# Optimization experiments

Hardware: AMD Instinct MI355X
Metric: run time of the kernel (lower is better)

The kernel has to match this reference:

```python
import jax, jax.numpy as jnp
import numpy as np

N = 50000      # nodes
E = 400000     # edges
IN = 128       # in_dim == emb_dim (residual requires equality)
POS = 64       # pos_in_dim
EMB = 128
LN_EPS = 1e-5


def _ln(x, g, b):
    m = jnp.mean(x, axis=-1, keepdims=True)
    v = jnp.mean((x - m) ** 2, axis=-1, keepdims=True)
    return (x - m) / jnp.sqrt(v + LN_EPS) * g + b


def _gin(x, src, dst, eps, W1, b1, g1, be1, W2, b2):
    # GINConv: mlp((1+eps)*x + sum_{j in N(i)} x_j)
    agg = jax.ops.segment_sum(x[src], dst, num_segments=x.shape[0])
    h = (1.0 + eps) * x + agg
    h = jax.nn.relu(_ln(h @ W1 + b1, g1, be1))
    return h @ W2 + b2


def setup_inputs() -> dict:
    key = jax.random.key(0)
    ks = jax.random.split(key, 8)
    x = jax.random.normal(ks[0], (N, IN), jnp.float32)
    pos = jax.random.normal(ks[1], (N, POS), jnp.float32)
    edge_index = jax.random.randint(ks[2], (2, E), 0, N)
    d = IN + POS
    f32 = jnp.float32
    W1 = (jax.random.normal(ks[3], (d, EMB), f32) / np.sqrt(d))
    W2 = (jax.random.normal(ks[4], (EMB, EMB), f32) / np.sqrt(EMB))
    W1p = (jax.random.normal(ks[5], (POS, EMB), f32) / np.sqrt(POS))
    W2p = (jax.random.normal(ks[6], (EMB, EMB), f32) / np.sqrt(EMB))
    z = jnp.zeros((EMB,), f32)
    o = jnp.ones((EMB,), f32)
    return {
        "x": x, "pos": pos, "edge_index": edge_index,
        "eps": jnp.zeros((), f32), "W1": W1, "b1": z, "g1": o, "be1": z,
        "W2": W2, "b2": z, "ln_g": o, "ln_b": z,
        "epsp": jnp.zeros((), f32), "W1p": W1p, "b1p": z, "g1p": o, "be1p": z,
        "W2p": W2p, "b2p": z, "lnp_g": o, "lnp_b": z,
    }


def reference(x, pos, edge_index, eps, W1, b1, g1, be1, W2, b2, ln_g, ln_b,
              epsp, W1p, b1p, g1p, be1p, W2p, b2p, lnp_g, lnp_b):
    src, dst = edge_index[0], edge_index[1]
    node_feats = jnp.concatenate([x, pos], axis=-1)  # [N, IN+POS]
    h = jax.nn.relu(_ln(_gin(node_feats, src, dst, eps, W1, b1, g1, be1, W2, b2), ln_g, ln_b))
    p = jax.nn.relu(_ln(_gin(pos, src, dst, epsp, W1p, b1p, g1p, be1p, W2p, b2p), lnp_g, lnp_b))
    # dropout is identity in eval mode (model_drop_ratio applied only when training)
    h = h + x  # add_residual=True
    return (h, p)
```

## Files before the change

### kernel.cpp

```cpp
#include <hip/hip_runtime.h>

#define NN    50000
#define NPAD  50048
#define HB    391
#define EE    400000
#define IND   128
#define POSD  64
#define DD    192
#define EMBD  128
#define LNEPS 1e-5f
#define CAP   32

#define CAT_B  4692
#define FILL_B 98
#define FILLV_B 391
#define WC_B   256

typedef __attribute__((ext_vector_type(8))) short bf16x8;
typedef __attribute__((ext_vector_type(4))) unsigned short u16x4;
typedef __attribute__((ext_vector_type(4))) float f32x4;
typedef unsigned short ushort_t;
typedef unsigned int uint_t;

#define MFMA16 __builtin_amdgcn_mfma_f32_16x16x32_bf16

__device__ inline ushort_t f2bf(float f) {
  union { float f; unsigned u; } v; v.f = f;
  unsigned r = (v.u + 0x7FFFu + ((v.u >> 16) & 1u)) >> 16;
  return (ushort_t)r;
}
__device__ inline float bf2f(unsigned u) {
  union { unsigned u; float f; } v; v.u = u << 16;
  return v.f;
}

__global__ __launch_bounds__(256) void prep_k(
    const float* __restrict__ x, const float* __restrict__ pos,
    const int* __restrict__ ei,
    const float* __restrict__ W1, const float* __restrict__ W2,
    const float* __restrict__ W1p, const float* __restrict__ W2p,
    int* __restrict__ cnt, int* __restrict__ csr,
    ushort_t* __restrict__ cat, ushort_t* __restrict__ wt) {
  const int bid = blockIdx.x;
  if (bid < FILLV_B) {
    int e0 = (bid * 256 + threadIdx.x) * 4;
    if (e0 >= EE) return;
    int4 s = *(const int4*)(ei + e0);
    int4 d = *(const int4*)(ei + EE + e0);
    int i0 = atomicAdd(&cnt[d.x], 1);
    int i1 = atomicAdd(&cnt[d.y], 1);
    int i2 = atomicAdd(&cnt[d.z], 1);
    int i3 = atomicAdd(&cnt[d.w], 1);
    if (i0 < CAP) csr[(size_t)d.x * CAP + i0] = s.x;
    if (i1 < CAP) csr[(size_t)d.y * CAP + i1] = s.y;
    if (i2 < CAP) csr[(size_t)d.z * CAP + i2] = s.z;
    if (i3 < CAP) csr[(size_t)d.w * CAP + i3] = s.w;
  } else if (bid < FILLV_B + CAT_B) {
    int id  = (bid - FILLV_B) * 256 + threadIdx.x;
    int n   = id / 24, sub = id - n * 24;
    bf16x8 o = (bf16x8){0, 0, 0, 0, 0, 0, 0, 0};
    if (n < NN) {
      const float* src = (sub < 16) ? (x + (size_t)n * IND + sub * 8)
                                    : (pos + (size_t)n * POSD + (sub - 16) * 8);
      f32x4 v0 = *(const f32x4*)(src);
      f32x4 v1 = *(const f32x4*)(src + 4);
#pragma unroll
      for (int i = 0; i < 4; ++i) {
        o[i]     = (short)f2bf(v0[i]);
        o[i + 4] = (short)f2bf(v1[i]);
      }
    }
    *(bf16x8*)(cat + (size_t)n * DD + sub * 8) = o;
  } else {
    int t = (bid - FILLV_B - CAT_B) * 256 + threadIdx.x;
    if (t < 24576) {
      int c = t / 192, k = t % 192;
      wt[t] = f2bf(W1[k * EMBD + c]);
    } else if (t < 40960) {
      int q = t - 24576; int c = q / 128, k = q % 128;
      wt[t] = f2bf(W2[k * EMBD + c]);
    } else if (t < 49152) {
      int q = t - 40960; int c = q / 64, k = q % 64;
      wt[t] = f2bf(W1p[k * EMBD + c]);
    } else {
      int q = t - 49152; int c = q / 128, k = q % 128;
      wt[t] = f2bf(W2p[k * EMBD + c]);
    }
  }
}

__global__ __launch_bounds__(256) void gather2_k(
    const ushort_t* __restrict__ cat, const int* __restrict__ cnt,
    const int* __restrict__ csr,
    const float* __restrict__ epsv, const float* __restrict__ epspv,
    ushort_t* __restrict__ h0, ushort_t* __restrict__ p0) {
  const int lane = threadIdx.x & 63;
  const int wv   = threadIdx.x >> 6;
  const int half = lane >> 5;
  const int l2   = lane & 31;
  const int n    = blockIdx.x * 8 + wv * 2 + half;

  int deg = 0;
  if (n < NN) { deg = cnt[n]; if (deg > CAP) deg = CAP; }
  int idx = (l2 < deg) ? csr[(size_t)n * CAP + l2] : NN;

  float a0 = 0.f, a1 = 0.f, a2 = 0.f, a3 = 0.f, a4 = 0.f, a5 = 0.f;
  for (int t = 0; t < deg; t += 8) {
    int s[8];
#pragma unroll
    for (int k = 0; k < 8; ++k) s[k] = __shfl(idx, half * 32 + t + k);
    u16x4 u[8]; uint_t v[8];
#pragma unroll
    for (int k = 0; k < 8; ++k) {
      int sk = (t + k < CAP) ? s[k] : NN;
      const ushort_t* r = cat + (size_t)sk * DD;
      u[k] = *(const u16x4*)(r + l2 * 4);
      v[k] = *(const uint_t*)(r + 128 + l2 * 2);
    }
#pragma unroll
    for (int k = 0; k < 8; ++k) {
      a0 += bf2f(u[k][0]); a1 += bf2f(u[k][1]);
      a2 += bf2f(u[k][2]); a3 += bf2f(u[k][3]);
      a4 += bf2f(v[k] & 0xffffu); a5 += bf2f(v[k] >> 16);
    }
  }

  const float e1  = 1.0f + epsv[0];
  const float ep1 = 1.0f + epspv[0];
  const ushort_t* self = cat + (size_t)n * DD;
  u16x4 su = *(const u16x4*)(self + l2 * 4);
  uint_t sv = *(const uint_t*)(self + 128 + l2 * 2);

  u16x4 o;
  o[0] = f2bf(fmaf(e1, bf2f(su[0]), a0));
  o[1] = f2bf(fmaf(e1, bf2f(su[1]), a1));
  o[2] = f2bf(fmaf(e1, bf2f(su[2]), a2));
  o[3] = f2bf(fmaf(e1, bf2f(su[3]), a3));
  *(u16x4*)(h0 + (size_t)n * DD + l2 * 4) = o;

  float p4 = bf2f(sv & 0xffffu), p5 = bf2f(sv >> 16);
  uint_t oh = (uint_t)f2bf(fmaf(e1, p4, a4)) |
              ((uint_t)f2bf(fmaf(e1, p5, a5)) << 16);
  *(uint_t*)(h0 + (size_t)n * DD + 128 + l2 * 2) = oh;
  uint_t op = (uint_t)f2bf(fmaf(ep1, p4, a4)) |
              ((uint_t)f2bf(fmaf(ep1, p5, a5)) << 16);
  *(uint_t*)(p0 + (size_t)n * POSD + l2 * 2) = op;
}

__device__ inline void ln_epi_T(f32x4 (&acc)[8][2],
                                const float* __restrict__ bias,
                                const float* __restrict__ gam,
                                const float* __restrict__ bet, int g) {
  f32x4 bv[8], gv[8], bev[8];
#pragma unroll
  for (int nt = 0; nt < 8; ++nt) {
    bv[nt]  = *(const f32x4*)(bias + nt * 16 + g * 4);
    gv[nt]  = *(const f32x4*)(gam  + nt * 16 + g * 4);
    bev[nt] = *(const f32x4*)(bet  + nt * 16 + g * 4);
  }
#pragma unroll
  for (int mt = 0; mt < 2; ++mt) {
    float s = 0.f, sq = 0.f;
#pragma unroll
    for (int nt = 0; nt < 8; ++nt)
#pragma unroll
      for (int r = 0; r < 4; ++r) {
        float v = acc[nt][mt][r] + bv[nt][r];
        acc[nt][mt][r] = v;
        s += v; sq += v * v;
      }
    s  += __shfl_xor(s, 16);  sq += __shfl_xor(sq, 16);
    s  += __shfl_xor(s, 32);  sq += __shfl_xor(sq, 32);
    float mean = s * (1.0f / 128.0f);
    float var  = sq * (1.0f / 128.0f) - mean * mean;
    float rstd = rsqrtf(var + LNEPS);
#pragma unroll
    for (int nt = 0; nt < 8; ++nt)
#pragma unroll
      for (int r = 0; r < 4; ++r)
        acc[nt][mt][r] = fmaxf(
            fmaf((acc[nt][mt][r] - mean) * rstd, gv[nt][r], bev[nt][r]), 0.f);
  }
}

__device__ inline void act_write_T(char* act, f32x4 (&acc)[8][2], int g, int c0) {
#pragma unroll
  for (int mt = 0; mt < 2; ++mt) {
    int lr = mt * 16 + c0;
    int sw = (lr & 7) << 4;
#pragma unroll
    for (int nt = 0; nt < 8; ++nt) {
      u16x4 o;
#pragma unroll
      for (int r = 0; r < 4; ++r) o[r] = f2bf(acc[nt][mt][r]);
      *(u16x4*)(act + lr * 256 + ((nt * 32 + g * 8) ^ sw)) = o;
    }
  }
}

__device__ inline void stage_w(const ushort_t* __restrict__ src, char* dst,
                               int rowbytes, int chunks, int tid) {
  int cpr = rowbytes >> 4;
  for (int i = tid; i < chunks; i += 256) {
    int row  = i / cpr;
    int colb = (i - row * cpr) << 4;
    *(bf16x8*)(dst + row * rowbytes + (colb ^ ((row & 7) << 4))) =
        *(const bf16x8*)(src + (size_t)i * 8);
  }
}

__global__ __launch_bounds__(256) void mlp_k(
    const ushort_t* __restrict__ h0, const ushort_t* __restrict__ p0,
    const ushort_t* __restrict__ wt,
    const float* __restrict__ b1, const float* __restrict__ g1,
    const float* __restrict__ be1,
    const float* __restrict__ b2, const float* __restrict__ lng,
    const float* __restrict__ lnb,
    const float* __restrict__ b1p, const float* __restrict__ g1p,
    const float* __restrict__ be1p,
    const float* __restrict__ b2p, const float* __restrict__ lnpg,
    const float* __restrict__ lnpb,
    const float* __restrict__ x, float* __restrict__ out) {
  __shared__ __align__(16) char smem[65536];
  const int tid  = threadIdx.x;
  const int lane = tid & 63;
  const int wv   = tid >> 6;
  const int g    = lane >> 4;
  const int c0   = lane & 15;
  const int bid  = blockIdx.x;
  char* act = smem + wv * 8192;

  f32x4 acc[8][2];

  if (bid < HB) {
    const int m0 = bid * 128;
    stage_w(wt, smem, 384, 3072, tid);
    bf16x8 a0[6], a1[6];
    const size_t r0 = (size_t)(m0 + wv * 32 + c0) * DD;
    const size_t r1 = r0 + (size_t)16 * DD;
#pragma unroll
    for (int ks = 0; ks < 6; ++ks) {
      a0[ks] = *(const bf16x8*)(h0 + r0 + ks * 32 + g * 8);
      a1[ks] = *(const bf16x8*)(h0 + r1 + ks * 32 + g * 8);
    }
    __syncthreads();

#pragma unroll
    for (int nt = 0; nt < 8; ++nt)
#pragma unroll
      for (int mt = 0; mt < 2; ++mt) acc[nt][mt] = (f32x4){0.f, 0.f, 0.f, 0.f};
#pragma unroll
    for (int ks = 0; ks < 6; ++ks)
#pragma unroll
      for (int nt = 0; nt < 8; ++nt) {
        int wrow = nt * 16 + c0;
        bf16x8 w = *(const bf16x8*)(smem + wrow * 384 +
                                    ((ks * 64 + g * 16) ^ ((wrow & 7) << 4)));
        acc[nt][0] = MFMA16(w, a0[ks], acc[nt][0], 0, 0, 0);
        acc[nt][1] = MFMA16(w, a1[ks], acc[nt][1], 0, 0, 0);
      }
    ln_epi_T(acc, b1, g1, be1, g);
    __syncthreads();
    act_write_T(act, acc, g, c0);
    stage_w(wt + 24576, smem + 32768, 256, 2048, tid);
    __syncthreads();

#pragma unroll
    for (int nt = 0; nt < 8; ++nt)
#pragma unroll
      for (int mt = 0; mt < 2; ++mt) acc[nt][mt] = (f32x4){0.f, 0.f, 0.f, 0.f};
#pragma unroll
    for (int ks = 0; ks < 4; ++ks) {
      bf16x8 am[2];
#pragma unroll
      for (int mt = 0; mt < 2; ++mt) {
        int lr = mt * 16 + c0;
        am[mt] = *(const bf16x8*)(act + lr * 256 +
                                  ((ks * 64 + g * 16) ^ ((lr & 7) << 4)));
      }
#pragma unroll
      for (int nt = 0; nt < 8; ++nt) {
        int wrow = nt * 16 + c0;
        bf16x8 w = *(const bf16x8*)(smem + 32768 + wrow * 256 +
                                    ((ks * 64 + g * 16) ^ ((wrow & 7) << 4)));
        acc[nt][0] = MFMA16(w, am[0], acc[nt][0], 0, 0, 0);
        acc[nt][1] = MFMA16(w, am[1], acc[nt][1], 0, 0, 0);
      }
    }
    ln_epi_T(acc, b2, lng, lnb, g);
#pragma unroll
    for (int mt = 0; mt < 2; ++mt) {
      int node = m0 + wv * 32 + mt * 16 + c0;
      if (node < NN) {
#pragma unroll
        for (int nt = 0; nt < 8; ++nt) {
          int f0 = nt * 16 + g * 4;
          f32x4 xr = *(const f32x4*)(x + (size_t)node * IND + f0);
          f32x4 o;
#pragma unroll
          for (int r = 0; r < 4; ++r) o[r] = acc[nt][mt][r] + xr[r];
          *(f32x4*)(out + (size_t)node * EMBD + f0) = o;
        }
      }
    }
  } else {
    const int m0 = (bid - HB) * 128;
    stage_w(wt + 40960, smem, 128, 1024, tid);
    bf16x8 a0[2], a1[2];
    const size_t r0 = (size_t)(m0 + wv * 32 + c0) * POSD;
    const size_t r1 = r0 + (size_t)16 * POSD;
#pragma unroll
    for (int ks = 0; ks < 2; ++ks) {
      a0[ks] = *(const bf16x8*)(p0 + r0 + ks * 32 + g * 8);
      a1[ks] = *(const bf16x8*)(p0 + r1 + ks * 32 + g * 8);
    }
    __syncthreads();

#pragma unroll
    for (int nt = 0; nt < 8; ++nt)
#pragma unroll
      for (int mt = 0; mt < 2; ++mt) acc[nt][mt] = (f32x4){0.f, 0.f, 0.f, 0.f};
#pragma unroll
    for (int ks = 0; ks < 2; ++ks)
#pragma unroll
      for (int nt = 0; nt < 8; ++nt) {
        int wrow = nt * 16 + c0;
        bf16x8 w = *(const bf16x8*)(smem + wrow * 128 +
                                    ((ks * 64 + g * 16) ^ ((wrow & 7) << 4)));
        acc[nt][0] = MFMA16(w, a0[ks], acc[nt][0], 0, 0, 0);
        acc[nt][1] = MFMA16(w, a1[ks], acc[nt][1], 0, 0, 0);
      }
    ln_epi_T(acc, b1p, g1p, be1p, g);
    __syncthreads();
    act_write_T(act, acc, g, c0);
    stage_w(wt + 49152, smem + 32768, 256, 2048, tid);
    __syncthreads();

#pragma unroll
    for (int nt = 0; nt < 8; ++nt)
#pragma unroll
      for (int mt = 0; mt < 2; ++mt) acc[nt][mt] = (f32x4){0.f, 0.f, 0.f, 0.f};
#pragma unroll
    for (int ks = 0; ks < 4; ++ks) {
      bf16x8 am[2];
#pragma unroll
      for (int mt = 0; mt < 2; ++mt) {
        int lr = mt * 16 + c0;
        am[mt] = *(const bf16x8*)(act + lr * 256 +
                                  ((ks * 64 + g * 16) ^ ((lr & 7) << 4)));
      }
#pragma unroll
      for (int nt = 0; nt < 8; ++nt) {
        int wrow = nt * 16 + c0;
        bf16x8 w = *(const bf16x8*)(smem + 32768 + wrow * 256 +
                                    ((ks * 64 + g * 16) ^ ((wrow & 7) << 4)));
        acc[nt][0] = MFMA16(w, am[0], acc[nt][0], 0, 0, 0);
        acc[nt][1] = MFMA16(w, am[1], acc[nt][1], 0, 0, 0);
      }
    }
    ln_epi_T(acc, b2p, lnpg, lnpb, g);
#pragma unroll
    for (int mt = 0; mt < 2; ++mt) {
      int node = m0 + wv * 32 + mt * 16 + c0;
      if (node < NN) {
#pragma unroll
        for (int nt = 0; nt < 8; ++nt) {
          int f0 = nt * 16 + g * 4;
          f32x4 o;
#pragma unroll
          for (int r = 0; r < 4; ++r) o[r] = acc[nt][mt][r];
          *(f32x4*)(out + (size_t)NN * EMBD + (size_t)node * EMBD + f0) = o;
        }
      }
    }
  }
}

extern "C" void kernel_launch(void* const* d_in, const int* in_sizes, int n_in,
                              void* d_out, int out_size, void* d_ws, size_t ws_size,
                              hipStream_t stream) {
  const float* x    = (const float*)d_in[0];
  const float* pos  = (const float*)d_in[1];
  const int*   ei   = (const int*)d_in[2];
  const float* eps  = (const float*)d_in[3];
  const float* W1   = (const float*)d_in[4];
  const float* b1   = (const float*)d_in[5];
  const float* g1   = (const float*)d_in[6];
  const float* be1  = (const float*)d_in[7];
  const float* W2   = (const float*)d_in[8];
  const float* b2   = (const float*)d_in[9];
  const float* lng  = (const float*)d_in[10];
  const float* lnb  = (const float*)d_in[11];
  const float* epsp = (const float*)d_in[12];
  const float* W1p  = (const float*)d_in[13];
  const float* b1p  = (const float*)d_in[14];
  const float* g1p  = (const float*)d_in[15];
  const float* be1p = (const float*)d_in[16];
  const float* W2p  = (const float*)d_in[17];
  const float* b2p  = (const float*)d_in[18];
  const float* lnpg = (const float*)d_in[19];
  const float* lnpb = (const float*)d_in[20];

  char* ws = (char*)d_ws;
  float* out = (float*)d_out;

  const size_t CATB = (size_t)NPAD * DD * 2;
  const size_t P0B  = (size_t)NPAD * POSD * 2;

  int*      cnt = (int*)ws;
  int*      csr = (int*)(ws + 200000);
  ushort_t* cat = (ushort_t*)(ws + 6600000);
  ushort_t* h0  = (ushort_t*)(ws + 6600000 + CATB);
  ushort_t* p0  = (ushort_t*)(ws + 6600000 + 2 * CATB);
  ushort_t* wt  = (ushort_t*)(ws + 6600000 + 2 * CATB + P0B);

  hipMemsetAsync(cnt, 0, (size_t)NN * sizeof(int), stream);
  prep_k<<<FILLV_B + CAT_B + WC_B, 256, 0, stream>>>(
      x, pos, ei, W1, W2, W1p, W2p, cnt, csr, cat, wt);
  gather2_k<<<NPAD / 8, 256, 0, stream>>>(cat, cnt, csr, eps, epsp, h0, p0);
  mlp_k<<<2 * HB, 256, 0, stream>>>(
      h0, p0, wt, b1, g1, be1, b2, lng, lnb,
      b1p, g1p, be1p, b2p, lnpg, lnpb, x, out);
}
```

Measured before the change: 111.8 us.

## Make MLP kernel persistent with both weight matrices staged once per block

```diff
diff --git a/kernel.cpp b/kernel.cpp
--- a/kernel.cpp
+++ b/kernel.cpp
@@ -2,7 +2,7 @@
 
 #define NN    50000
 #define NPAD  50048
-#define HB    391
+#define NT32  1564
 #define EE    400000
 #define IND   128
 #define POSD  64
@@ -11,10 +11,9 @@
 #define LNEPS 1e-5f
 #define CAP   32
 
-#define CAT_B  4692
-#define FILL_B 98
 #define FILLV_B 391
-#define WC_B   256
+#define CAT_B   4692
+#define WC_B    256
 
 typedef __attribute__((ext_vector_type(8))) short bf16x8;
 typedef __attribute__((ext_vector_type(4))) unsigned short u16x4;
@@ -199,9 +198,9 @@
 }
 
 __device__ inline void stage_w(const ushort_t* __restrict__ src, char* dst,
-                               int rowbytes, int chunks, int tid) {
+                               int rowbytes, int chunks, int tid, int stride) {
   int cpr = rowbytes >> 4;
-  for (int i = tid; i < chunks; i += 256) {
+  for (int i = tid; i < chunks; i += stride) {
     int row  = i / cpr;
     int colb = (i - row * cpr) << 4;
     *(bf16x8*)(dst + row * rowbytes + (colb ^ ((row & 7) << 4))) =
@@ -209,7 +208,7 @@
   }
 }
 
-__global__ __launch_bounds__(256) void mlp_k(
+__global__ __launch_bounds__(512) void mlp_persist_k(
     const ushort_t* __restrict__ h0, const ushort_t* __restrict__ p0,
     const ushort_t* __restrict__ wt,
     const float* __restrict__ b1, const float* __restrict__ g1,
@@ -221,155 +220,155 @@
     const float* __restrict__ b2p, const float* __restrict__ lnpg,
     const float* __restrict__ lnpb,
     const float* __restrict__ x, float* __restrict__ out) {
-  __shared__ __align__(16) char smem[65536];
+  __shared__ __align__(16) char smem[147456];
   const int tid  = threadIdx.x;
   const int lane = tid & 63;
   const int wv   = tid >> 6;
   const int g    = lane >> 4;
   const int c0   = lane & 15;
   const int bid  = blockIdx.x;
-  char* act = smem + wv * 8192;
+  char* act = smem + 81920 + wv * 8192;
 
   f32x4 acc[8][2];
 
-  if (bid < HB) {
-    const int m0 = bid * 128;
-    stage_w(wt, smem, 384, 3072, tid);
-    bf16x8 a0[6], a1[6];
-    const size_t r0 = (size_t)(m0 + wv * 32 + c0) * DD;
-    const size_t r1 = r0 + (size_t)16 * DD;
-#pragma unroll
-    for (int ks = 0; ks < 6; ++ks) {
-      a0[ks] = *(const bf16x8*)(h0 + r0 + ks * 32 + g * 8);
-      a1[ks] = *(const bf16x8*)(h0 + r1 + ks * 32 + g * 8);
-    }
+  if (bid < 128) {
+    stage_w(wt, smem, 384, 3072, tid, 512);
+    stage_w(wt + 24576, smem + 49152, 256, 2048, tid, 512);
     __syncthreads();
 
-#pragma unroll
-    for (int nt = 0; nt < 8; ++nt)
-#pragma unroll
-      for (int mt = 0; mt < 2; ++mt) acc[nt][mt] = (f32x4){0.f, 0.f, 0.f, 0.f};
-#pragma unroll
-    for (int ks = 0; ks < 6; ++ks)
-#pragma unroll
-      for (int nt = 0; nt < 8; ++nt) {
-        int wrow = nt * 16 + c0;
-        bf16x8 w = *(const bf16x8*)(smem + wrow * 384 +
-                                    ((ks * 64 + g * 16) ^ ((wrow & 7) << 4)));
-        acc[nt][0] = MFMA16(w, a0[ks], acc[nt][0], 0, 0, 0);
-        acc[nt][1] = MFMA16(w, a1[ks], acc[nt][1], 0, 0, 0);
-      }
-    ln_epi_T(acc, b1, g1, be1, g);
+    for (int t = bid * 8 + wv; t < NT32; t += 1024) {
+      const int row0 = t * 32;
+      bf16x8 a0[6], a1[6];
+      const size_t r0 = (size_t)(row0 + c0) * DD;
+      const size_t r1 = r0 + (size_t)16 * DD;
+#pragma unroll
+      for (int ks = 0; ks < 6; ++ks) {
+        a0[ks] = *(const bf16x8*)(h0 + r0 + ks * 32 + g * 8);
+        a1[ks] = *(const bf16x8*)(h0 + r1 + ks * 32 + g * 8);
+      }
+#pragma unroll
+      for (int nt = 0; nt < 8; ++nt)
+#pragma unroll
+        for (int mt = 0; mt < 2; ++mt) acc[nt][mt] = (f32x4){0.f, 0.f, 0.f, 0.f};
+#pragma unroll
+      for (int ks = 0; ks < 6; ++ks)
+#pragma unroll
+        for (int nt = 0; nt < 8; ++nt) {
+          int wrow = nt * 16 + c0;
+          bf16x8 w = *(const bf16x8*)(smem + wrow * 384 +
+                                      ((ks * 64 + g * 16) ^ ((wrow & 7) << 4)));
+          acc[nt][0] = MFMA16(w, a0[ks], acc[nt][0], 0, 0, 0);
+          acc[nt][1] = MFMA16(w, a1[ks], acc[nt][1], 0, 0, 0);
+        }
+      ln_epi_T(acc, b1, g1, be1, g);
+      act_write_T(act, acc, g, c0);
+
+#pragma unroll
+      for (int nt = 0; nt < 8; ++nt)
+#pragma unroll
+        for (int mt = 0; mt < 2; ++mt) acc[nt][mt] = (f32x4){0.f, 0.f, 0.f, 0.f};
+#pragma unroll
+      for (int ks = 0; ks < 4; ++ks) {
+        bf16x8 am[2];
+#pragma unroll
+        for (int mt = 0; mt < 2; ++mt) {
+          int lr = mt * 16 + c0;
+          am[mt] = *(const bf16x8*)(act + lr * 256 +
+                                    ((ks * 64 + g * 16) ^ ((lr & 7) << 4)));
+        }
+#pragma unroll
+        for (int nt = 0; nt < 8; ++nt) {
+          int wrow = nt * 16 + c0;
+          bf16x8 w = *(const bf16x8*)(smem + 49152 + wrow * 256 +
+                                      ((ks * 64 + g * 16) ^ ((wrow & 7) << 4)));
+          acc[nt][0] = MFMA16(w, am[0], acc[nt][0], 0, 0, 0);
+          acc[nt][1] = MFMA16(w, am[1], acc[nt][1], 0, 0, 0);
+        }
+      }
+      ln_epi_T(acc, b2, lng, lnb, g);
+#pragma unroll
+      for (int mt = 0; mt < 2; ++mt) {
+        int node = row0 + mt * 16 + c0;
+        if (node < NN) {
+#pragma unroll
+          for (int nt = 0; nt < 8; ++nt) {
+            int f0 = nt * 16 + g * 4;
+            f32x4 xr = *(const f32x4*)(x + (size_t)node * IND + f0);
+            f32x4 o;
+#pragma unroll
+            for (int r = 0; r < 4; ++r) o[r] = acc[nt][mt][r] + xr[r];
+            *(f32x4*)(out + (size_t)node * EMBD + f0) = o;
+          }
+        }
+      }
+    }
+  } else {
+    stage_w(wt + 40960, smem, 128, 1024, tid, 512);
+    stage_w(wt + 49152, smem + 16384, 256, 2048, tid, 512);
     __syncthreads();
-    act_write_T(act, acc, g, c0);
-    stage_w(wt + 24576, smem + 32768, 256, 2048, tid);
-    __syncthreads();
-
-#pragma unroll
-    for (int nt = 0; nt < 8; ++nt)
-#pragma unroll
-      for (int mt = 0; mt < 2; ++mt) acc[nt][mt] = (f32x4){0.f, 0.f, 0.f, 0.f};
-#pragma unroll
-    for (int ks = 0; ks < 4; ++ks) {
-      bf16x8 am[2];
+
+    for (int t = (bid - 128) * 8 + wv; t < NT32; t += 1024) {
+      const int row0 = t * 32;
+      bf16x8 a0[2], a1[2];
+      const size_t r0 = (size_t)(row0 + c0) * POSD;
+      const size_t r1 = r0 + (size_t)16 * POSD;
+#pragma unroll
+      for (int ks = 0; ks < 2; ++ks) {
+        a0[ks] = *(const bf16x8*)(p0 + r0 + ks * 32 + g * 8);
+        a1[ks] = *(const bf16x8*)(p0 + r1 + ks * 32 + g * 8);
+      }
+#pragma unroll
+      for (int nt = 0; nt < 8; ++nt)
+#pragma unroll
+        for (int mt = 0; mt < 2; ++mt) acc[nt][mt] = (f32x4){0.f, 0.f, 0.f, 0.f};
+#pragma unroll
+      for (int ks = 0; ks < 2; ++ks)
+#pragma unroll
+        for (int nt = 0; nt < 8; ++nt) {
+          int wrow = nt * 16 + c0;
+          bf16x8 w = *(const bf16x8*)(smem + wrow * 128 +
+                                      ((ks * 64 + g * 16) ^ ((wrow & 7) << 4)));
+          acc[nt][0] = MFMA16(w, a0[ks], acc[nt][0], 0, 0, 0);
+          acc[nt][1] = MFMA16(w, a1[ks], acc[nt][1], 0, 0, 0);
+        }
+      ln_epi_T(acc, b1p, g1p, be1p, g);
+      act_write_T(act, acc, g, c0);
+
+#pragma unroll
+      for (int nt = 0; nt < 8; ++nt)
+#pragma unroll
+        for (int mt = 0; mt < 2; ++mt) acc[nt][mt] = (f32x4){0.f, 0.f, 0.f, 0.f};
+#pragma unroll
+      for (int ks = 0; ks < 4; ++ks) {
+        bf16x8 am[2];
+#pragma unroll
+        for (int mt = 0; mt < 2; ++mt) {
+          int lr = mt * 16 + c0;
+          am[mt] = *(const bf16x8*)(act + lr * 256 +
+                                    ((ks * 64 + g * 16) ^ ((lr & 7) << 4)));
+        }
+#pragma unroll
+        for (int nt = 0; nt < 8; ++nt) {
+          int wrow = nt * 16 + c0;
+          bf16x8 w = *(const bf16x8*)(smem + 16384 + wrow * 256 +
+                                      ((ks * 64 + g * 16) ^ ((wrow & 7) << 4)));
+          acc[nt][0] = MFMA16(w, am[0], acc[nt][0], 0, 0, 0);
+          acc[nt][1] = MFMA16(w, am[1], acc[nt][1], 0, 0, 0);
+        }
+      }
+      ln_epi_T(acc, b2p, lnpg, lnpb, g);
 #pragma unroll
       for (int mt = 0; mt < 2; ++mt) {
-        int lr = mt * 16 + c0;
-        am[mt] = *(const bf16x8*)(act + lr * 256 +
-                                  ((ks * 64 + g * 16) ^ ((lr & 7) << 4)));
-      }
-#pragma unroll
-      for (int nt = 0; nt < 8; ++nt) {
-        int wrow = nt * 16 + c0;
-        bf16x8 w = *(const bf16x8*)(smem + 32768 + wrow * 256 +
-                                    ((ks * 64 + g * 16) ^ ((wrow & 7) << 4)));
-        acc[nt][0] = MFMA16(w, am[0], acc[nt][0], 0, 0, 0);
-        acc[nt][1] = MFMA16(w, am[1], acc[nt][1], 0, 0, 0);
-      }
-    }
-    ln_epi_T(acc, b2, lng, lnb, g);
-#pragma unroll
-    for (int mt = 0; mt < 2; ++mt) {
-      int node = m0 + wv * 32 + mt * 16 + c0;
-      if (node < NN) {
-#pragma unroll
-        for (int nt = 0; nt < 8; ++nt) {
-          int f0 = nt * 16 + g * 4;
-          f32x4 xr = *(const f32x4*)(x + (size_t)node * IND + f0);
-          f32x4 o;
-#pragma unroll
-          for (int r = 0; r < 4; ++r) o[r] = acc[nt][mt][r] + xr[r];
-          *(f32x4*)(out + (size_t)node * EMBD + f0) = o;
-        }
-      }
-    }
-  } else {
-    const int m0 = (bid - HB) * 128;
-    stage_w(wt + 40960, smem, 128, 1024, tid);
-    bf16x8 a0[2], a1[2];
-    const size_t r0 = (size_t)(m0 + wv * 32 + c0) * POSD;
-    const size_t r1 = r0 + (size_t)16 * POSD;
-#pragma unroll
-    for (int ks = 0; ks < 2; ++ks) {
-      a0[ks] = *(const bf16x8*)(p0 + r0 + ks * 32 + g * 8);
-      a1[ks] = *(const bf16x8*)(p0 + r1 + ks * 32 + g * 8);
-    }
-    __syncthreads();
-
-#pragma unroll
-    for (int nt = 0; nt < 8; ++nt)
-#pragma unroll
-      for (int mt = 0; mt < 2; ++mt) acc[nt][mt] = (f32x4){0.f, 0.f, 0.f, 0.f};
-#pragma unroll
-    for (int ks = 0; ks < 2; ++ks)
-#pragma unroll
-      for (int nt = 0; nt < 8; ++nt) {
-        int wrow = nt * 16 + c0;
-        bf16x8 w = *(const bf16x8*)(smem + wrow * 128 +
-                                    ((ks * 64 + g * 16) ^ ((wrow & 7) << 4)));
-        acc[nt][0] = MFMA16(w, a0[ks], acc[nt][0], 0, 0, 0);
-        acc[nt][1] = MFMA16(w, a1[ks], acc[nt][1], 0, 0, 0);
-      }
-    ln_epi_T(acc, b1p, g1p, be1p, g);
-    __syncthreads();
-    act_write_T(act, acc, g, c0);
-    stage_w(wt + 49152, smem + 32768, 256, 2048, tid);
-    __syncthreads();
-
-#pragma unroll
-    for (int nt = 0; nt < 8; ++nt)
-#pragma unroll
-      for (int mt = 0; mt < 2; ++mt) acc[nt][mt] = (f32x4){0.f, 0.f, 0.f, 0.f};
-#pragma unroll
-    for (int ks = 0; ks < 4; ++ks) {
-      bf16x8 am[2];
-#pragma unroll
-      for (int mt = 0; mt < 2; ++mt) {
-        int lr = mt * 16 + c0;
-        am[mt] = *(const bf16x8*)(act + lr * 256 +
-                                  ((ks * 64 + g * 16) ^ ((lr & 7) << 4)));
-      }
-#pragma unroll
-      for (int nt = 0; nt < 8; ++nt) {
-        int wrow = nt * 16 + c0;
-        bf16x8 w = *(const bf16x8*)(smem + 32768 + wrow * 256 +
-                                    ((ks * 64 + g * 16) ^ ((wrow & 7) << 4)));
-        acc[nt][0] = MFMA16(w, am[0], acc[nt][0], 0, 0, 0);
-        acc[nt][1] = MFMA16(w, am[1], acc[nt][1], 0, 0, 0);
-      }
-    }
-    ln_epi_T(acc, b2p, lnpg, lnpb, g);
-#pragma unroll
-    for (int mt = 0; mt < 2; ++mt) {
-      int node = m0 + wv * 32 + mt * 16 + c0;
-      if (node < NN) {
-#pragma unroll
-        for (int nt = 0; nt < 8; ++nt) {
-          int f0 = nt * 16 + g * 4;
-          f32x4 o;
-#pragma unroll
-          for (int r = 0; r < 4; ++r) o[r] = acc[nt][mt][r];
-          *(f32x4*)(out + (size_t)NN * EMBD + (size_t)node * EMBD + f0) = o;
+        int node = row0 + mt * 16 + c0;
+        if (node < NN) {
+#pragma unroll
+          for (int nt = 0; nt < 8; ++nt) {
+            int f0 = nt * 16 + g * 4;
+            f32x4 o;
+#pragma unroll
+            for (int r = 0; r < 4; ++r) o[r] = acc[nt][mt][r];
+            *(f32x4*)(out + (size_t)NN * EMBD + (size_t)node * EMBD + f0) = o;
+          }
         }
       }
     }
@@ -418,7 +417,7 @@
   prep_k<<<FILLV_B + CAT_B + WC_B, 256, 0, stream>>>(
       x, pos, ei, W1, W2, W1p, W2p, cnt, csr, cat, wt);
   gather2_k<<<NPAD / 8, 256, 0, stream>>>(cat, cnt, csr, eps, epsp, h0, p0);
-  mlp_k<<<2 * HB, 256, 0, stream>>>(
+  mlp_persist_k<<<256, 512, 0, stream>>>(
       h0, p0, wt, b1, g1, be1, b2, lng, lnb,
       b1p, g1p, be1p, b2p, lnpg, lnpb, x, out);
 }
```

Result: slower. 129.4 us (+15.7%).

## Stage both MLP weight matrices up front via direct global-to-LDS loads

Applied to the files above, without the earlier changes.

```diff
diff --git a/kernel.cpp b/kernel.cpp
--- a/kernel.cpp
+++ b/kernel.cpp
@@ -11,10 +11,9 @@
 #define LNEPS 1e-5f
 #define CAP   32
 
-#define CAT_B  4692
-#define FILL_B 98
 #define FILLV_B 391
-#define WC_B   256
+#define CAT_B   4692
+#define WC_B    256
 
 typedef __attribute__((ext_vector_type(8))) short bf16x8;
 typedef __attribute__((ext_vector_type(4))) unsigned short u16x4;
@@ -198,8 +197,24 @@
   }
 }
 
+#if __has_builtin(__builtin_amdgcn_global_load_lds)
 __device__ inline void stage_w(const ushort_t* __restrict__ src, char* dst,
-                               int rowbytes, int chunks, int tid) {
+                               int rowbytes, int chunks, int tid, int wv) {
+  int cpr = rowbytes >> 4;
+  for (int k = 0; k < chunks; k += 256) {
+    int c    = k + tid;
+    int row  = c / cpr;
+    int colb = ((c - row * cpr) << 4) ^ ((row & 7) << 4);
+    const char* g = (const char*)src + row * rowbytes + colb;
+    char* l = dst + (k + (wv << 6)) * 16;
+    __builtin_amdgcn_global_load_lds(
+        (const __attribute__((address_space(1))) void*)g,
+        (__attribute__((address_space(3))) void*)l, 16, 0, 0);
+  }
+}
+#else
+__device__ inline void stage_w(const ushort_t* __restrict__ src, char* dst,
+                               int rowbytes, int chunks, int tid, int wv) {
   int cpr = rowbytes >> 4;
   for (int i = tid; i < chunks; i += 256) {
     int row  = i / cpr;
@@ -208,6 +223,7 @@
         *(const bf16x8*)(src + (size_t)i * 8);
   }
 }
+#endif
 
 __global__ __launch_bounds__(256) void mlp_k(
     const ushort_t* __restrict__ h0, const ushort_t* __restrict__ p0,
@@ -221,20 +237,20 @@
     const float* __restrict__ b2p, const float* __restrict__ lnpg,
     const float* __restrict__ lnpb,
     const float* __restrict__ x, float* __restrict__ out) {
-  __shared__ __align__(16) char smem[65536];
+  __shared__ __align__(16) char smem[81920];
   const int tid  = threadIdx.x;
   const int lane = tid & 63;
   const int wv   = tid >> 6;
   const int g    = lane >> 4;
   const int c0   = lane & 15;
   const int bid  = blockIdx.x;
-  char* act = smem + wv * 8192;
 
   f32x4 acc[8][2];
 
   if (bid < HB) {
     const int m0 = bid * 128;
-    stage_w(wt, smem, 384, 3072, tid);
+    stage_w(wt, smem, 384, 3072, tid, wv);
+    stage_w(wt + 24576, smem + 49152, 256, 2048, tid, wv);
     bf16x8 a0[6], a1[6];
     const size_t r0 = (size_t)(m0 + wv * 32 + c0) * DD;
     const size_t r1 = r0 + (size_t)16 * DD;
@@ -261,9 +277,9 @@
       }
     ln_epi_T(acc, b1, g1, be1, g);
     __syncthreads();
+
+    char* act = smem + wv * 8192;
     act_write_T(act, acc, g, c0);
-    stage_w(wt + 24576, smem + 32768, 256, 2048, tid);
-    __syncthreads();
 
 #pragma unroll
     for (int nt = 0; nt < 8; ++nt)
@@ -281,7 +297,7 @@
 #pragma unroll
       for (int nt = 0; nt < 8; ++nt) {
         int wrow = nt * 16 + c0;
-        bf16x8 w = *(const bf16x8*)(smem + 32768 + wrow * 256 +
+        bf16x8 w = *(const bf16x8*)(smem + 49152 + wrow * 256 +
                                     ((ks * 64 + g * 16) ^ ((wrow & 7) << 4)));
         acc[nt][0] = MFMA16(w, am[0], acc[nt][0], 0, 0, 0);
         acc[nt][1] = MFMA16(w, am[1], acc[nt][1], 0, 0, 0);
@@ -305,7 +321,8 @@
     }
   } else {
     const int m0 = (bid - HB) * 128;
-    stage_w(wt + 40960, smem, 128, 1024, tid);
+    stage_w(wt + 40960, smem, 128, 1024, tid, wv);
+    stage_w(wt + 49152, smem + 16384, 256, 2048, tid, wv);
     bf16x8 a0[2], a1[2];
     const size_t r0 = (size_t)(m0 + wv * 32 + c0) * POSD;
     const size_t r1 = r0 + (size_t)16 * POSD;
@@ -331,10 +348,9 @@
         acc[nt][1] = MFMA16(w, a1[ks], acc[nt][1], 0, 0, 0);
       }
     ln_epi_T(acc, b1p, g1p, be1p, g);
-    __syncthreads();
+
+    char* act = smem + 49152 + wv * 8192;
     act_write_T(act, acc, g, c0);
-    stage_w(wt + 49152, smem + 32768, 256, 2048, tid);
-    __syncthreads();
 
 #pragma unroll
     for (int nt = 0; nt < 8; ++nt)
@@ -352,7 +368,7 @@
 #pragma unroll
       for (int nt = 0; nt < 8; ++nt) {
         int wrow = nt * 16 + c0;
-        bf16x8 w = *(const bf16x8*)(smem + 32768 + wrow * 256 +
+        bf16x8 w = *(const bf16x8*)(smem + 16384 + wrow * 256 +
                                     ((ks * 64 + g * 16) ^ ((wrow & 7) << 4)));
         acc[nt][0] = MFMA16(w, am[0], acc[nt][0], 0, 0, 0);
         acc[nt][1] = MFMA16(w, am[1], acc[nt][1], 0, 0, 0);
```

After: 105.1 us (median of 2 runs). -6.0%, faster.
